# Performance work log

Hardware: AMD Instinct MI355X
Metric: run time of the kernel (lower is better)

## Reference

```python
import jax, jax.numpy as jnp
import numpy as np

N_NODES = 100000
N_EDGES = 500000
N_RELS = 200
N_BASE = 50
INIT_D = 100
FEAT_D = 128
N_CLS = 50
N_LAYERS = 2
BN_EPS = 1e-5


def setup_inputs() -> dict:
    key = jax.random.key(0)
    ks = jax.random.split(key, 16)
    inp = {
        'edge_src': jax.random.randint(ks[0], (N_LAYERS, N_EDGES), 0, N_NODES),
        'edge_dst': jax.random.randint(ks[1], (N_LAYERS, N_EDGES), 0, N_NODES),
        'edge_type': jax.random.randint(ks[2], (N_LAYERS, N_EDGES), 0, N_RELS),
        'emb_h': jax.random.normal(ks[3], (N_NODES, INIT_D), jnp.float32),
        'emb_e': jax.random.normal(ks[4], (N_BASE, INIT_D), jnp.float32),
        'rel_wt': jax.random.normal(ks[5], (N_RELS, N_BASE), jnp.float32) * 0.1,
        'W_h_init': jax.random.normal(ks[6], (INIT_D, FEAT_D), jnp.float32) * (1.0 / np.sqrt(INIT_D)),
        'W_e_init': jax.random.normal(ks[7], (INIT_D, FEAT_D), jnp.float32) * (1.0 / np.sqrt(INIT_D)),
        'aggre_W': jax.random.normal(ks[8], (FEAT_D, FEAT_D), jnp.float32) * (1.0 / np.sqrt(FEAT_D)),
        'aggre_b': jnp.zeros((FEAT_D,), jnp.float32),
        'bn_gamma': jnp.ones((FEAT_D,), jnp.float32),
        'bn_beta': jnp.zeros((FEAT_D,), jnp.float32),
        'fc0_w': jax.random.normal(ks[9], (FEAT_D, FEAT_D // 2), jnp.float32) * (1.0 / np.sqrt(FEAT_D)),
        'fc0_b': jnp.zeros((FEAT_D // 2,), jnp.float32),
        'fc1_w': jax.random.normal(ks[10], (FEAT_D // 2, FEAT_D // 4), jnp.float32) * (1.0 / np.sqrt(FEAT_D // 2)),
        'fc1_b': jnp.zeros((FEAT_D // 4,), jnp.float32),
        'fc2_w': jax.random.normal(ks[11], (FEAT_D // 4, N_CLS), jnp.float32) * (1.0 / np.sqrt(FEAT_D // 4)),
        'fc2_b': jnp.zeros((N_CLS,), jnp.float32),
    }
    return inp


def _segment_mean(msg, dst, num_segments):
    # mean reduction of per-edge messages into dst nodes (DGL reduce_mean)
    sums = jax.ops.segment_sum(msg, dst, num_segments=num_segments)
    cnt = jax.ops.segment_sum(jnp.ones((msg.shape[0], 1), msg.dtype), dst,
                              num_segments=num_segments)
    return sums / jnp.maximum(cnt, 1.0)


def _forward(emb_h, emb_e, rel_wt, W_h_init, W_e_init, aggre_W, aggre_b,
             bn_gamma, bn_beta, fc0_w, fc0_b, fc1_w, fc1_b, fc2_w, fc2_b,
             edge_src, edge_dst, edge_type):
    node_embed = None
    for i in range(N_LAYERS):
        src, dst, etype = edge_src[i], edge_dst[i], edge_type[i]
        if i == 0:
            # embedding gather + init projection: [E, init_d] @ [init_d, feat]
            src_emb = emb_h[src] @ W_h_init
        else:
            src_emb = node_embed[src]
        # relation-weight mixing: rel_wt[etype] @ emb_e, then init projection
        edges_embed = (rel_wt[etype] @ emb_e) @ W_e_init  # [E, feat]
        # message = relu(linear(src)) composed with relation embedding
        msg = jax.nn.relu(src_emb @ aggre_W + aggre_b) + edges_embed
        node_embed = _segment_mean(msg, dst, N_NODES)
    # batchnorm over node dim (training batch stats)
    mu = jnp.mean(node_embed, axis=0)
    var = jnp.var(node_embed, axis=0)
    h = (node_embed - mu) * jax.lax.rsqrt(var + BN_EPS) * bn_gamma + bn_beta
    h = jax.nn.relu(h)
    # MLP classifier: 128 -> 64 -> 32 -> num_classes
    h = jax.nn.relu(h @ fc0_w + fc0_b)
    h = jax.nn.relu(h @ fc1_w + fc1_b)
    logits = h @ fc2_w + fc2_b
    return logits


def reference(edge_src, edge_dst, edge_type, emb_h, emb_e, rel_wt, W_h_init,
              W_e_init, aggre_W, aggre_b, bn_gamma, bn_beta, fc0_w, fc0_b,
              fc1_w, fc1_b, fc2_w, fc2_b):
    return _forward(emb_h, emb_e, rel_wt, W_h_init, W_e_init, aggre_W,
                    aggre_b, bn_gamma, bn_beta, fc0_w, fc0_b, fc1_w, fc1_b,
                    fc2_w, fc2_b, edge_src, edge_dst, edge_type)
```

## Files before the change

### kernel.cpp

```cpp
#include <hip/hip_runtime.h>
#include <cstdint>
#include <cstddef>

#define N_NODES 100000
#define N_EDGES 500000
#define N_RELS  200
#define N_BASE  50
#define INIT_D  100
#define FEAT_D  128
#define N_CLS   50
#define BN_EPS  1e-5f

#define SCAN_BLK 1024
#define NB_SCAN  ((N_NODES + SCAN_BLK - 1) / SCAN_BLK)

typedef unsigned int uint;
typedef unsigned short ushort;

__device__ inline uint packbf2(float a, float b) {
  uint ua = __float_as_uint(a); ua = (ua + 0x7fffu + ((ua >> 16) & 1u)) >> 16;
  uint ub = __float_as_uint(b); ub = (ub + 0x7fffu + ((ub >> 16) & 1u)) >> 16;
  return ua | (ub << 16);
}
__device__ inline float bf_lo(uint u) { return __uint_as_float(u << 16); }
__device__ inline float bf_hi(uint u) { return __uint_as_float(u & 0xffff0000u); }

__global__ __launch_bounds__(128)
void rel_kernel(const float* __restrict__ rel_wt, const float* __restrict__ emb_e,
                const float* __restrict__ W_e, float* __restrict__ REL) {
  int r = blockIdx.x;
  int t = threadIdx.x;
  __shared__ float T[INIT_D];
  if (t < INIT_D) {
    float a = 0.f;
    for (int b = 0; b < N_BASE; ++b)
      a += rel_wt[r * N_BASE + b] * emb_e[b * INIT_D + t];
    T[t] = a;
  }
  __syncthreads();
  float a = 0.f;
  for (int k = 0; k < INIT_D; ++k)
    a += T[k] * W_e[k * FEAT_D + t];
  REL[r * FEAT_D + t] = a;
}

__global__ __launch_bounds__(128)
void wcomb_kernel(const float* __restrict__ W_h, const float* __restrict__ aggre_W,
                  float* __restrict__ WC) {
  int i = blockIdx.x;
  int j = threadIdx.x;
  __shared__ float row[FEAT_D];
  row[j] = W_h[i * FEAT_D + j];
  __syncthreads();
  float a = 0.f;
  for (int f = 0; f < FEAT_D; ++f)
    a += row[f] * aggre_W[f * FEAT_D + j];
  WC[i * FEAT_D + j] = a;
}

__global__ __launch_bounds__(256)
void h0_kernel(const float* __restrict__ emb_h, const float* __restrict__ WC,
               const float* __restrict__ bias, ushort* __restrict__ H, int nNodes) {
  __shared__ float WT[FEAT_D * INIT_D];
  __shared__ float bs[FEAT_D];
  int t = threadIdx.x;
  for (int i = t; i < FEAT_D * INIT_D; i += 256) {
    int k = i >> 7, j = i & 127;
    WT[j * INIT_D + k] = WC[i];
  }
  if (t < FEAT_D) bs[t] = bias[t];
  __syncthreads();
  for (int n = blockIdx.x * 256 + t; n < nNodes; n += gridDim.x * 256) {
    float x[INIT_D];
    const float4* xp = (const float4*)(emb_h + (size_t)n * INIT_D);
#pragma unroll
    for (int q = 0; q < 25; ++q) {
      float4 v = xp[q];
      x[4 * q + 0] = v.x; x[4 * q + 1] = v.y; x[4 * q + 2] = v.z; x[4 * q + 3] = v.w;
    }
    uint2* orow = (uint2*)(H + (size_t)n * FEAT_D);
    for (int j4 = 0; j4 < 32; ++j4) {
      float4 a;
      a.x = bs[4 * j4 + 0]; a.y = bs[4 * j4 + 1];
      a.z = bs[4 * j4 + 2]; a.w = bs[4 * j4 + 3];
      const float4* w0 = (const float4*)&WT[(4 * j4 + 0) * INIT_D];
      const float4* w1 = (const float4*)&WT[(4 * j4 + 1) * INIT_D];
      const float4* w2 = (const float4*)&WT[(4 * j4 + 2) * INIT_D];
      const float4* w3 = (const float4*)&WT[(4 * j4 + 3) * INIT_D];
#pragma unroll
      for (int q = 0; q < 25; ++q) {
        float4 v0 = w0[q], v1 = w1[q], v2 = w2[q], v3 = w3[q];
        a.x = fmaf(x[4*q+0], v0.x, a.x); a.x = fmaf(x[4*q+1], v0.y, a.x);
        a.x = fmaf(x[4*q+2], v0.z, a.x); a.x = fmaf(x[4*q+3], v0.w, a.x);
        a.y = fmaf(x[4*q+0], v1.x, a.y); a.y = fmaf(x[4*q+1], v1.y, a.y);
        a.y = fmaf(x[4*q+2], v1.z, a.y); a.y = fmaf(x[4*q+3], v1.w, a.y);
        a.z = fmaf(x[4*q+0], v2.x, a.z); a.z = fmaf(x[4*q+1], v2.y, a.z);
        a.z = fmaf(x[4*q+2], v2.z, a.z); a.z = fmaf(x[4*q+3], v2.w, a.z);
        a.w = fmaf(x[4*q+0], v3.x, a.w); a.w = fmaf(x[4*q+1], v3.y, a.w);
        a.w = fmaf(x[4*q+2], v3.z, a.w); a.w = fmaf(x[4*q+3], v3.w, a.w);
      }
      a.x = fmaxf(a.x, 0.f); a.y = fmaxf(a.y, 0.f);
      a.z = fmaxf(a.z, 0.f); a.w = fmaxf(a.w, 0.f);
      uint2 pk; pk.x = packbf2(a.x, a.y); pk.y = packbf2(a.z, a.w);
      orow[j4] = pk;
    }
  }
}

__global__ __launch_bounds__(256)
void hist_kernel(const int* __restrict__ dst, int* __restrict__ deg, int nEdges) {
  for (int e = blockIdx.x * 256 + threadIdx.x; e < nEdges; e += gridDim.x * 256)
    atomicAdd(&deg[dst[e]], 1);
}

__global__ __launch_bounds__(256)
void scanA_kernel(const int* __restrict__ deg, int* __restrict__ bsum, int n) {
  __shared__ int red[256];
  int t = threadIdx.x;
  int base = blockIdx.x * SCAN_BLK + t * 4;
  int s = 0;
#pragma unroll
  for (int q = 0; q < 4; ++q) {
    int i = base + q;
    s += (i < n) ? deg[i] : 0;
  }
  red[t] = s;
  __syncthreads();
  for (int off = 128; off > 0; off >>= 1) {
    if (t < off) red[t] += red[t + off];
    __syncthreads();
  }
  if (t == 0) bsum[blockIdx.x] = red[0];
}

__global__ void scanB_kernel(int* __restrict__ bsum, int nb, int* __restrict__ off) {
  int run = 0;
  for (int i = 0; i < nb; ++i) {
    int v = bsum[i];
    bsum[i] = run;
    run += v;
  }
  off[N_NODES] = run;
}

__global__ __launch_bounds__(256)
void scanC_kernel(const int* __restrict__ deg, const int* __restrict__ bsum,
                  int* __restrict__ off, int* __restrict__ cur, int n) {
  __shared__ int lds[256];
  int t = threadIdx.x;
  int base = blockIdx.x * SCAN_BLK + t * 4;
  int d[4];
  int s = 0;
#pragma unroll
  for (int q = 0; q < 4; ++q) {
    int i = base + q;
    d[q] = (i < n) ? deg[i] : 0;
    s += d[q];
  }
  lds[t] = s;
  __syncthreads();
  for (int o = 1; o < 256; o <<= 1) {
    int v = (t >= o) ? lds[t - o] : 0;
    __syncthreads();
    lds[t] += v;
    __syncthreads();
  }
  int excl = lds[t] - s + bsum[blockIdx.x];
#pragma unroll
  for (int q = 0; q < 4; ++q) {
    int i = base + q;
    if (i < n) {
      off[i] = excl;
      cur[i] = excl;
    }
    excl += d[q];
  }
}

__global__ __launch_bounds__(256)
void fill_kernel(const int* __restrict__ src, const int* __restrict__ dst,
                 const int* __restrict__ et, int* __restrict__ cur,
                 int* __restrict__ epk, int nEdges) {
  for (int e = blockIdx.x * 256 + threadIdx.x; e < nEdges; e += gridDim.x * 256) {
    int d = dst[e];
    int pos = atomicAdd(&cur[d], 1);
    epk[pos] = src[e] | (et[e] << 17);
  }
}

__global__ __launch_bounds__(256)
void gather_mean_kernel(const int* __restrict__ off, const int* __restrict__ epk,
                        const ushort* __restrict__ H, const float* __restrict__ REL,
                        float* __restrict__ MEAN, int doBN, float* __restrict__ acc,
                        int nNodes) {
  const uint2* H2 = (const uint2*)H;
  const float4* R4 = (const float4*)REL;
  float4* M4 = (float4*)MEAN;
  int t = threadIdx.x;
  int j = t & 31;
  int slot = t >> 5;
  float4 s1 = {0.f, 0.f, 0.f, 0.f}, s2 = {0.f, 0.f, 0.f, 0.f};
  for (int n = blockIdx.x * 8 + slot; n < nNodes; n += gridDim.x * 8) {
    int beg = off[n], end = off[n + 1];
    float4 a = {0.f, 0.f, 0.f, 0.f};
    int p = beg;
#pragma unroll 1
    for (; p + 4 <= end; p += 4) {
      int u0 = epk[p + 0];
      int u1 = epk[p + 1];
      int u2 = epk[p + 2];
      int u3 = epk[p + 3];
      uint2 h0 = H2[(size_t)(u0 & 0x1FFFF) * 32 + j];
      uint2 h1 = H2[(size_t)(u1 & 0x1FFFF) * 32 + j];
      uint2 h2 = H2[(size_t)(u2 & 0x1FFFF) * 32 + j];
      uint2 h3 = H2[(size_t)(u3 & 0x1FFFF) * 32 + j];
      float4 r0 = R4[(u0 >> 17) * 32 + j];
      float4 r1 = R4[(u1 >> 17) * 32 + j];
      float4 r2 = R4[(u2 >> 17) * 32 + j];
      float4 r3 = R4[(u3 >> 17) * 32 + j];
      a.x += (bf_lo(h0.x) + r0.x) + (bf_lo(h1.x) + r1.x) +
             (bf_lo(h2.x) + r2.x) + (bf_lo(h3.x) + r3.x);
      a.y += (bf_hi(h0.x) + r0.y) + (bf_hi(h1.x) + r1.y) +
             (bf_hi(h2.x) + r2.y) + (bf_hi(h3.x) + r3.y);
      a.z += (bf_lo(h0.y) + r0.z) + (bf_lo(h1.y) + r1.z) +
             (bf_lo(h2.y) + r2.z) + (bf_lo(h3.y) + r3.z);
      a.w += (bf_hi(h0.y) + r0.w) + (bf_hi(h1.y) + r1.w) +
             (bf_hi(h2.y) + r2.w) + (bf_hi(h3.y) + r3.w);
    }
#pragma unroll 1
    for (; p < end; ++p) {
      int u = epk[p];
      uint2 hv = H2[(size_t)(u & 0x1FFFF) * 32 + j];
      float4 rv = R4[(u >> 17) * 32 + j];
      a.x += bf_lo(hv.x) + rv.x; a.y += bf_hi(hv.x) + rv.y;
      a.z += bf_lo(hv.y) + rv.z; a.w += bf_hi(hv.y) + rv.w;
    }
    float rd = (end > beg) ? 1.f / (float)(end - beg) : 0.f;
    a.x *= rd; a.y *= rd; a.z *= rd; a.w *= rd;
    M4[(size_t)n * 32 + j] = a;
    if (doBN) {
      s1.x += a.x; s1.y += a.y; s1.z += a.z; s1.w += a.w;
      s2.x += a.x * a.x; s2.y += a.y * a.y;
      s2.z += a.z * a.z; s2.w += a.w * a.w;
    }
  }
  if (doBN) {
    __shared__ float4 r1[8][32], r2[8][32];
    r1[slot][j] = s1;
    r2[slot][j] = s2;
    __syncthreads();
    if (slot == 0) {
      float4 a1 = r1[0][j], a2 = r2[0][j];
#pragma unroll
      for (int k = 1; k < 8; ++k) {
        float4 b1 = r1[k][j], b2 = r2[k][j];
        a1.x += b1.x; a1.y += b1.y; a1.z += b1.z; a1.w += b1.w;
        a2.x += b2.x; a2.y += b2.y; a2.z += b2.z; a2.w += b2.w;
      }
      atomicAdd(&acc[4 * j + 0], a1.x);
      atomicAdd(&acc[4 * j + 1], a1.y);
      atomicAdd(&acc[4 * j + 2], a1.z);
      atomicAdd(&acc[4 * j + 3], a1.w);
      atomicAdd(&acc[FEAT_D + 4 * j + 0], a2.x);
      atomicAdd(&acc[FEAT_D + 4 * j + 1], a2.y);
      atomicAdd(&acc[FEAT_D + 4 * j + 2], a2.z);
      atomicAdd(&acc[FEAT_D + 4 * j + 3], a2.w);
    }
  }
}

__global__ __launch_bounds__(256)
void h1_kernel(const float* __restrict__ mean, const float* __restrict__ W,
               const float* __restrict__ bias, ushort* __restrict__ H, int nNodes) {
  __shared__ float WT[FEAT_D * FEAT_D];
  __shared__ float bs[FEAT_D];
  int t = threadIdx.x;
  for (int i = t; i < FEAT_D * FEAT_D; i += 256) {
    int k = i >> 7, j = i & 127;
    WT[j * FEAT_D + k] = W[i];
  }
  if (t < FEAT_D) bs[t] = bias[t];
  __syncthreads();
  for (int n = blockIdx.x * 256 + t; n < nNodes; n += gridDim.x * 256) {
    float x[FEAT_D];
    const float4* xp = (const float4*)(mean + (size_t)n * FEAT_D);
#pragma unroll
    for (int q = 0; q < 32; ++q) {
      float4 v = xp[q];
      x[4 * q + 0] = v.x; x[4 * q + 1] = v.y;
      x[4 * q + 2] = v.z; x[4 * q + 3] = v.w;
    }
    uint2* orow = (uint2*)(H + (size_t)n * FEAT_D);
    for (int j4 = 0; j4 < 32; ++j4) {
      float4 a;
      a.x = bs[4 * j4 + 0]; a.y = bs[4 * j4 + 1];
      a.z = bs[4 * j4 + 2]; a.w = bs[4 * j4 + 3];
      const float4* w0 = (const float4*)&WT[(4 * j4 + 0) * FEAT_D];
      const float4* w1 = (const float4*)&WT[(4 * j4 + 1) * FEAT_D];
      const float4* w2 = (const float4*)&WT[(4 * j4 + 2) * FEAT_D];
      const float4* w3 = (const float4*)&WT[(4 * j4 + 3) * FEAT_D];
#pragma unroll
      for (int q = 0; q < 32; ++q) {
        float4 v0 = w0[q], v1 = w1[q], v2 = w2[q], v3 = w3[q];
        a.x = fmaf(x[4*q+0], v0.x, a.x); a.x = fmaf(x[4*q+1], v0.y, a.x);
        a.x = fmaf(x[4*q+2], v0.z, a.x); a.x = fmaf(x[4*q+3], v0.w, a.x);
        a.y = fmaf(x[4*q+0], v1.x, a.y); a.y = fmaf(x[4*q+1], v1.y, a.y);
        a.y = fmaf(x[4*q+2], v1.z, a.y); a.y = fmaf(x[4*q+3], v1.w, a.y);
        a.z = fmaf(x[4*q+0], v2.x, a.z); a.z = fmaf(x[4*q+1], v2.y, a.z);
        a.z = fmaf(x[4*q+2], v2.z, a.z); a.z = fmaf(x[4*q+3], v2.w, a.z);
        a.w = fmaf(x[4*q+0], v3.x, a.w); a.w = fmaf(x[4*q+1], v3.y, a.w);
        a.w = fmaf(x[4*q+2], v3.z, a.w); a.w = fmaf(x[4*q+3], v3.w, a.w);
      }
      a.x = fmaxf(a.x, 0.f); a.y = fmaxf(a.y, 0.f);
      a.z = fmaxf(a.z, 0.f); a.w = fmaxf(a.w, 0.f);
      uint2 pk; pk.x = packbf2(a.x, a.y); pk.y = packbf2(a.z, a.w);
      orow[j4] = pk;
    }
  }
}

__global__ __launch_bounds__(256)
void final_kernel(const float* __restrict__ mean, const float* __restrict__ acc,
                  const float* __restrict__ gamma, const float* __restrict__ beta,
                  const float* __restrict__ fc0w, const float* __restrict__ fc0b,
                  const float* __restrict__ fc1w, const float* __restrict__ fc1b,
                  const float* __restrict__ fc2w, const float* __restrict__ fc2b,
                  float* __restrict__ out, int nNodes) {
  __shared__ float W0T[64 * FEAT_D];
  __shared__ float W1L[64 * 32];
  __shared__ float W2T[N_CLS * 32];
  __shared__ float sc[FEAT_D], sh[FEAT_D];
  __shared__ float b0[64], b1[32], b2[N_CLS];
  int t = threadIdx.x;
  for (int i = t; i < 64 * FEAT_D; i += 256) {
    int k = i >> 6, j = i & 63;
    W0T[j * FEAT_D + k] = fc0w[i];
  }
  for (int i = t; i < 64 * 32; i += 256) W1L[i] = fc1w[i];
  for (int i = t; i < 32 * N_CLS; i += 256) {
    int jj = i / N_CLS, c = i % N_CLS;
    W2T[c * 32 + jj] = fc2w[i];
  }
  if (t < FEAT_D) {
    float m = acc[t] * (1.f / (float)N_NODES);
    float v = acc[FEAT_D + t] * (1.f / (float)N_NODES) - m * m;
    float r = rsqrtf(v + BN_EPS);
    float g = gamma[t];
    sc[t] = r * g;
    sh[t] = beta[t] - m * r * g;
  }
  if (t < 64) b0[t] = fc0b[t];
  if (t < 32) b1[t] = fc1b[t];
  if (t < N_CLS) b2[t] = fc2b[t];
  __syncthreads();
  for (int n = blockIdx.x * 256 + t; n < nNodes; n += gridDim.x * 256) {
    float x[FEAT_D];
    const float4* xp = (const float4*)(mean + (size_t)n * FEAT_D);
#pragma unroll
    for (int q = 0; q < 32; ++q) {
      float4 v = xp[q];
      x[4*q+0] = fmaxf(fmaf(v.x, sc[4*q+0], sh[4*q+0]), 0.f);
      x[4*q+1] = fmaxf(fmaf(v.y, sc[4*q+1], sh[4*q+1]), 0.f);
      x[4*q+2] = fmaxf(fmaf(v.z, sc[4*q+2], sh[4*q+2]), 0.f);
      x[4*q+3] = fmaxf(fmaf(v.w, sc[4*q+3], sh[4*q+3]), 0.f);
    }
    float acc2[32];
#pragma unroll
    for (int jj = 0; jj < 32; ++jj) acc2[jj] = b1[jj];
    for (int j = 0; j < 64; ++j) {
      float a = b0[j];
      const float4* w = (const float4*)&W0T[j * FEAT_D];
#pragma unroll
      for (int q = 0; q < 32; ++q) {
        float4 v = w[q];
        a = fmaf(x[4*q+0], v.x, a); a = fmaf(x[4*q+1], v.y, a);
        a = fmaf(x[4*q+2], v.z, a); a = fmaf(x[4*q+3], v.w, a);
      }
      float h = fmaxf(a, 0.f);
      const float4* w1 = (const float4*)&W1L[j * 32];
#pragma unroll
      for (int q = 0; q < 8; ++q) {
        float4 v = w1[q];
        acc2[4*q+0] = fmaf(h, v.x, acc2[4*q+0]);
        acc2[4*q+1] = fmaf(h, v.y, acc2[4*q+1]);
        acc2[4*q+2] = fmaf(h, v.z, acc2[4*q+2]);
        acc2[4*q+3] = fmaf(h, v.w, acc2[4*q+3]);
      }
    }
    float h2[32];
#pragma unroll
    for (int jj = 0; jj < 32; ++jj) h2[jj] = fmaxf(acc2[jj], 0.f);
    float* orow = out + (size_t)n * N_CLS;
    for (int cc = 0; cc < N_CLS; ++cc) {
      float a = b2[cc];
      const float4* w = (const float4*)&W2T[cc * 32];
#pragma unroll
      for (int q = 0; q < 8; ++q) {
        float4 v = w[q];
        a = fmaf(h2[4*q+0], v.x, a); a = fmaf(h2[4*q+1], v.y, a);
        a = fmaf(h2[4*q+2], v.z, a); a = fmaf(h2[4*q+3], v.w, a);
      }
      orow[cc] = a;
    }
  }
}

extern "C" void kernel_launch(void* const* d_in, const int* in_sizes, int n_in,
                              void* d_out, int out_size, void* d_ws, size_t ws_size,
                              hipStream_t stream) {
  const int* edge_src = (const int*)d_in[0];
  const int* edge_dst = (const int*)d_in[1];
  const int* edge_type = (const int*)d_in[2];
  const float* emb_h = (const float*)d_in[3];
  const float* emb_e = (const float*)d_in[4];
  const float* rel_wt = (const float*)d_in[5];
  const float* W_h_init = (const float*)d_in[6];
  const float* W_e_init = (const float*)d_in[7];
  const float* aggre_W = (const float*)d_in[8];
  const float* aggre_b = (const float*)d_in[9];
  const float* bn_gamma = (const float*)d_in[10];
  const float* bn_beta = (const float*)d_in[11];
  const float* fc0_w = (const float*)d_in[12];
  const float* fc0_b = (const float*)d_in[13];
  const float* fc1_w = (const float*)d_in[14];
  const float* fc1_b = (const float*)d_in[15];
  const float* fc2_w = (const float*)d_in[16];
  const float* fc2_b = (const float*)d_in[17];
  float* out = (float*)d_out;

  char* ws = (char*)d_ws;
  float*  REL  = (float*)(ws);
  float*  WC   = (float*)(ws + 102400);
  ushort* H    = (ushort*)(ws + 153600);
  float*  MEAN = (float*)(ws + 25753600);
  float*  ACC  = (float*)(ws + 76953600);

  char* ob = (char*)d_out;
  int* EPK  = (int*)(ob);
  int* DEG  = (int*)(ob + 2000000);
  int* OFF  = (int*)(ob + 2400000);
  int* CUR  = (int*)(ob + 2800004);
  int* BSUM = (int*)(ob + 3200008);

  const int NODE_BLOCKS = (N_NODES + 255) / 256;
  const int GATHER_BLOCKS = 2048;

  hipMemsetAsync(ACC, 0, 1024, stream);

  rel_kernel<<<N_RELS, 128, 0, stream>>>(rel_wt, emb_e, W_e_init, REL);
  wcomb_kernel<<<INIT_D, 128, 0, stream>>>(W_h_init, aggre_W, WC);
  h0_kernel<<<NODE_BLOCKS, 256, 0, stream>>>(emb_h, WC, aggre_b, H, N_NODES);

  hipMemsetAsync(DEG, 0, 400000, stream);
  hist_kernel<<<1024, 256, 0, stream>>>(edge_dst, DEG, N_EDGES);
  scanA_kernel<<<NB_SCAN, 256, 0, stream>>>(DEG, BSUM, N_NODES);
  scanB_kernel<<<1, 1, 0, stream>>>(BSUM, NB_SCAN, OFF);
  scanC_kernel<<<NB_SCAN, 256, 0, stream>>>(DEG, BSUM, OFF, CUR, N_NODES);
  fill_kernel<<<1024, 256, 0, stream>>>(edge_src, edge_dst, edge_type, CUR, EPK,
                                        N_EDGES);
  gather_mean_kernel<<<GATHER_BLOCKS, 256, 0, stream>>>(OFF, EPK, H, REL, MEAN, 0,
                                                        ACC, N_NODES);

  h1_kernel<<<NODE_BLOCKS, 256, 0, stream>>>(MEAN, aggre_W, aggre_b, H, N_NODES);

  hipMemsetAsync(DEG, 0, 400000, stream);
  hist_kernel<<<1024, 256, 0, stream>>>(edge_dst + N_EDGES, DEG, N_EDGES);
  scanA_kernel<<<NB_SCAN, 256, 0, stream>>>(DEG, BSUM, N_NODES);
  scanB_kernel<<<1, 1, 0, stream>>>(BSUM, NB_SCAN, OFF);
  scanC_kernel<<<NB_SCAN, 256, 0, stream>>>(DEG, BSUM, OFF, CUR, N_NODES);
  fill_kernel<<<1024, 256, 0, stream>>>(edge_src + N_EDGES, edge_dst + N_EDGES,
                                        edge_type + N_EDGES, CUR, EPK, N_EDGES);
  gather_mean_kernel<<<GATHER_BLOCKS, 256, 0, stream>>>(OFF, EPK, H, REL, MEAN, 1,
                                                        ACC, N_NODES);

  final_kernel<<<NODE_BLOCKS, 256, 0, stream>>>(MEAN, ACC, bn_gamma, bn_beta,
                                                fc0_w, fc0_b, fc1_w, fc1_b,
                                                fc2_w, fc2_b, out, N_NODES);
}
```

Baseline: 760.6 us.

## Merge setup kernels, fold memsets into node kernels, parallelize block scan, nontemporal I/O

Merges the relation-embedding and weight-combination kernels into one launch. The DEG and ACC zeroing moves into h0_kernel and h1_kernel, which removes the hipMemsetAsync calls. The serial single-thread block-sum scan becomes a 128-thread shared-memory scan. Streaming stores and loads of MEAN and the output become nontemporal, and the gather grid is doubled. Together these cut launch count and serial latency, at the cost of relying on kernel ordering for the zeroing.

```diff
diff --git a/kernel.cpp b/kernel.cpp
--- a/kernel.cpp
+++ b/kernel.cpp
@@ -16,6 +16,7 @@
 
 typedef unsigned int uint;
 typedef unsigned short ushort;
+typedef float f4v __attribute__((ext_vector_type(4)));
 
 __device__ inline uint packbf2(float a, float b) {
   uint ua = __float_as_uint(a); ua = (ua + 0x7fffu + ((ua >> 16) & 1u)) >> 16;
@@ -26,44 +27,48 @@
 __device__ inline float bf_hi(uint u) { return __uint_as_float(u & 0xffff0000u); }
 
 __global__ __launch_bounds__(128)
-void rel_kernel(const float* __restrict__ rel_wt, const float* __restrict__ emb_e,
-                const float* __restrict__ W_e, float* __restrict__ REL) {
-  int r = blockIdx.x;
-  int t = threadIdx.x;
-  __shared__ float T[INIT_D];
-  if (t < INIT_D) {
+void relwc_kernel(const float* __restrict__ rel_wt, const float* __restrict__ emb_e,
+                  const float* __restrict__ W_e, float* __restrict__ REL,
+                  const float* __restrict__ W_h, const float* __restrict__ aggre_W,
+                  float* __restrict__ WC) {
+  __shared__ float T[FEAT_D];
+  int t = threadIdx.x;
+  if (blockIdx.x < N_RELS) {
+    int r = blockIdx.x;
+    if (t < INIT_D) {
+      float a = 0.f;
+      for (int b = 0; b < N_BASE; ++b)
+        a += rel_wt[r * N_BASE + b] * emb_e[b * INIT_D + t];
+      T[t] = a;
+    }
+    __syncthreads();
     float a = 0.f;
-    for (int b = 0; b < N_BASE; ++b)
-      a += rel_wt[r * N_BASE + b] * emb_e[b * INIT_D + t];
-    T[t] = a;
-  }
-  __syncthreads();
-  float a = 0.f;
-  for (int k = 0; k < INIT_D; ++k)
-    a += T[k] * W_e[k * FEAT_D + t];
-  REL[r * FEAT_D + t] = a;
-}
-
-__global__ __launch_bounds__(128)
-void wcomb_kernel(const float* __restrict__ W_h, const float* __restrict__ aggre_W,
-                  float* __restrict__ WC) {
-  int i = blockIdx.x;
-  int j = threadIdx.x;
-  __shared__ float row[FEAT_D];
-  row[j] = W_h[i * FEAT_D + j];
-  __syncthreads();
-  float a = 0.f;
-  for (int f = 0; f < FEAT_D; ++f)
-    a += row[f] * aggre_W[f * FEAT_D + j];
-  WC[i * FEAT_D + j] = a;
+    for (int k = 0; k < INIT_D; ++k)
+      a += T[k] * W_e[k * FEAT_D + t];
+    REL[r * FEAT_D + t] = a;
+  } else {
+    int i = blockIdx.x - N_RELS;
+    T[t] = W_h[i * FEAT_D + t];
+    __syncthreads();
+    float a = 0.f;
+    for (int f = 0; f < FEAT_D; ++f)
+      a += T[f] * aggre_W[f * FEAT_D + t];
+    WC[i * FEAT_D + t] = a;
+  }
 }
 
 __global__ __launch_bounds__(256)
 void h0_kernel(const float* __restrict__ emb_h, const float* __restrict__ WC,
-               const float* __restrict__ bias, ushort* __restrict__ H, int nNodes) {
+               const float* __restrict__ bias, ushort* __restrict__ H,
+               int* __restrict__ deg, float* __restrict__ acc, int nNodes) {
   __shared__ float WT[FEAT_D * INIT_D];
   __shared__ float bs[FEAT_D];
   int t = threadIdx.x;
+  {
+    int g = blockIdx.x * 256 + t;
+    if (g < N_NODES) deg[g] = 0;
+    if (g < 2 * FEAT_D) acc[g] = 0.f;
+  }
   for (int i = t; i < FEAT_D * INIT_D; i += 256) {
     int k = i >> 7, j = i & 127;
     WT[j * INIT_D + k] = WC[i];
@@ -133,14 +138,21 @@
   if (t == 0) bsum[blockIdx.x] = red[0];
 }
 
-__global__ void scanB_kernel(int* __restrict__ bsum, int nb, int* __restrict__ off) {
-  int run = 0;
-  for (int i = 0; i < nb; ++i) {
-    int v = bsum[i];
-    bsum[i] = run;
-    run += v;
-  }
-  off[N_NODES] = run;
+__global__ __launch_bounds__(128)
+void scanBw_kernel(int* __restrict__ bsum, int nb, int* __restrict__ off) {
+  __shared__ int s[128];
+  int t = threadIdx.x;
+  int v = (t < nb) ? bsum[t] : 0;
+  s[t] = v;
+  __syncthreads();
+  for (int o = 1; o < 128; o <<= 1) {
+    int u = (t >= o) ? s[t - o] : 0;
+    __syncthreads();
+    s[t] += u;
+    __syncthreads();
+  }
+  if (t < nb) bsum[t] = s[t] - v;
+  if (t == nb - 1) off[N_NODES] = s[t];
 }
 
 __global__ __launch_bounds__(256)
@@ -195,7 +207,6 @@
                         int nNodes) {
   const uint2* H2 = (const uint2*)H;
   const float4* R4 = (const float4*)REL;
-  float4* M4 = (float4*)MEAN;
   int t = threadIdx.x;
   int j = t & 31;
   int slot = t >> 5;
@@ -237,7 +248,8 @@
     }
     float rd = (end > beg) ? 1.f / (float)(end - beg) : 0.f;
     a.x *= rd; a.y *= rd; a.z *= rd; a.w *= rd;
-    M4[(size_t)n * 32 + j] = a;
+    f4v m; m[0] = a.x; m[1] = a.y; m[2] = a.z; m[3] = a.w;
+    __builtin_nontemporal_store(m, (f4v*)(MEAN + (size_t)n * FEAT_D) + j);
     if (doBN) {
       s1.x += a.x; s1.y += a.y; s1.z += a.z; s1.w += a.w;
       s2.x += a.x * a.x; s2.y += a.y * a.y;
@@ -271,10 +283,15 @@
 
 __global__ __launch_bounds__(256)
 void h1_kernel(const float* __restrict__ mean, const float* __restrict__ W,
-               const float* __restrict__ bias, ushort* __restrict__ H, int nNodes) {
+               const float* __restrict__ bias, ushort* __restrict__ H,
+               int* __restrict__ deg, int nNodes) {
   __shared__ float WT[FEAT_D * FEAT_D];
   __shared__ float bs[FEAT_D];
   int t = threadIdx.x;
+  {
+    int g = blockIdx.x * 256 + t;
+    if (g < N_NODES) deg[g] = 0;
+  }
   for (int i = t; i < FEAT_D * FEAT_D; i += 256) {
     int k = i >> 7, j = i & 127;
     WT[j * FEAT_D + k] = W[i];
@@ -283,12 +300,12 @@
   __syncthreads();
   for (int n = blockIdx.x * 256 + t; n < nNodes; n += gridDim.x * 256) {
     float x[FEAT_D];
-    const float4* xp = (const float4*)(mean + (size_t)n * FEAT_D);
+    const f4v* xp = (const f4v*)(mean + (size_t)n * FEAT_D);
 #pragma unroll
     for (int q = 0; q < 32; ++q) {
-      float4 v = xp[q];
-      x[4 * q + 0] = v.x; x[4 * q + 1] = v.y;
-      x[4 * q + 2] = v.z; x[4 * q + 3] = v.w;
+      f4v v = __builtin_nontemporal_load(xp + q);
+      x[4 * q + 0] = v[0]; x[4 * q + 1] = v[1];
+      x[4 * q + 2] = v[2]; x[4 * q + 3] = v[3];
     }
     uint2* orow = (uint2*)(H + (size_t)n * FEAT_D);
     for (int j4 = 0; j4 < 32; ++j4) {
@@ -355,14 +372,14 @@
   __syncthreads();
   for (int n = blockIdx.x * 256 + t; n < nNodes; n += gridDim.x * 256) {
     float x[FEAT_D];
-    const float4* xp = (const float4*)(mean + (size_t)n * FEAT_D);
+    const f4v* xp = (const f4v*)(mean + (size_t)n * FEAT_D);
 #pragma unroll
     for (int q = 0; q < 32; ++q) {
-      float4 v = xp[q];
-      x[4*q+0] = fmaxf(fmaf(v.x, sc[4*q+0], sh[4*q+0]), 0.f);
-      x[4*q+1] = fmaxf(fmaf(v.y, sc[4*q+1], sh[4*q+1]), 0.f);
-      x[4*q+2] = fmaxf(fmaf(v.z, sc[4*q+2], sh[4*q+2]), 0.f);
-      x[4*q+3] = fmaxf(fmaf(v.w, sc[4*q+3], sh[4*q+3]), 0.f);
+      f4v v = __builtin_nontemporal_load(xp + q);
+      x[4*q+0] = fmaxf(fmaf(v[0], sc[4*q+0], sh[4*q+0]), 0.f);
+      x[4*q+1] = fmaxf(fmaf(v[1], sc[4*q+1], sh[4*q+1]), 0.f);
+      x[4*q+2] = fmaxf(fmaf(v[2], sc[4*q+2], sh[4*q+2]), 0.f);
+      x[4*q+3] = fmaxf(fmaf(v[3], sc[4*q+3], sh[4*q+3]), 0.f);
     }
     float acc2[32];
 #pragma unroll
@@ -400,7 +417,7 @@
         a = fmaf(h2[4*q+0], v.x, a); a = fmaf(h2[4*q+1], v.y, a);
         a = fmaf(h2[4*q+2], v.z, a); a = fmaf(h2[4*q+3], v.w, a);
       }
-      orow[cc] = a;
+      __builtin_nontemporal_store(a, &orow[cc]);
     }
   }
 }
@@ -443,30 +460,28 @@
   int* BSUM = (int*)(ob + 3200008);
 
   const int NODE_BLOCKS = (N_NODES + 255) / 256;
-  const int GATHER_BLOCKS = 2048;
-
-  hipMemsetAsync(ACC, 0, 1024, stream);
-
-  rel_kernel<<<N_RELS, 128, 0, stream>>>(rel_wt, emb_e, W_e_init, REL);
-  wcomb_kernel<<<INIT_D, 128, 0, stream>>>(W_h_init, aggre_W, WC);
-  h0_kernel<<<NODE_BLOCKS, 256, 0, stream>>>(emb_h, WC, aggre_b, H, N_NODES);
-
-  hipMemsetAsync(DEG, 0, 400000, stream);
+  const int GATHER_BLOCKS = 4096;
+
+  relwc_kernel<<<N_RELS + INIT_D, 128, 0, stream>>>(rel_wt, emb_e, W_e_init, REL,
+                                                    W_h_init, aggre_W, WC);
+  h0_kernel<<<NODE_BLOCKS, 256, 0, stream>>>(emb_h, WC, aggre_b, H, DEG, ACC,
+                                             N_NODES);
+
   hist_kernel<<<1024, 256, 0, stream>>>(edge_dst, DEG, N_EDGES);
   scanA_kernel<<<NB_SCAN, 256, 0, stream>>>(DEG, BSUM, N_NODES);
-  scanB_kernel<<<1, 1, 0, stream>>>(BSUM, NB_SCAN, OFF);
+  scanBw_kernel<<<1, 128, 0, stream>>>(BSUM, NB_SCAN, OFF);
   scanC_kernel<<<NB_SCAN, 256, 0, stream>>>(DEG, BSUM, OFF, CUR, N_NODES);
   fill_kernel<<<1024, 256, 0, stream>>>(edge_src, edge_dst, edge_type, CUR, EPK,
                                         N_EDGES);
   gather_mean_kernel<<<GATHER_BLOCKS, 256, 0, stream>>>(OFF, EPK, H, REL, MEAN, 0,
                                                         ACC, N_NODES);
 
-  h1_kernel<<<NODE_BLOCKS, 256, 0, stream>>>(MEAN, aggre_W, aggre_b, H, N_NODES);
-
-  hipMemsetAsync(DEG, 0, 400000, stream);
+  h1_kernel<<<NODE_BLOCKS, 256, 0, stream>>>(MEAN, aggre_W, aggre_b, H, DEG,
+                                             N_NODES);
+
   hist_kernel<<<1024, 256, 0, stream>>>(edge_dst + N_EDGES, DEG, N_EDGES);
   scanA_kernel<<<NB_SCAN, 256, 0, stream>>>(DEG, BSUM, N_NODES);
-  scanB_kernel<<<1, 1, 0, stream>>>(BSUM, NB_SCAN, OFF);
+  scanBw_kernel<<<1, 128, 0, stream>>>(BSUM, NB_SCAN, OFF);
   scanC_kernel<<<NB_SCAN, 256, 0, stream>>>(DEG, BSUM, OFF, CUR, N_NODES);
   fill_kernel<<<1024, 256, 0, stream>>>(edge_src + N_EDGES, edge_dst + N_EDGES,
                                         edge_type + N_EDGES, CUR, EPK, N_EDGES);
```

After: 1.030 ms. 1.35x slower.
